# Kernel tuning notes

Hardware: AMD Instinct MI355X
Metric: run time of the kernel (lower is better)

The kernel has to match this reference:

```python
import jax, jax.numpy as jnp
import numpy as np
import math

D_MODEL = 1024
N_HEADS = 16
HEAD_DIM = D_MODEL // N_HEADS
B, S = 4, 4096


def setup_inputs() -> dict:
    key = jax.random.key(0)
    ks = jax.random.split(key, 8)
    # xavier-uniform-ish scale for square DxD matrices
    lim = math.sqrt(6.0 / (D_MODEL + D_MODEL))
    def W(k):
        return jax.random.uniform(k, (D_MODEL, D_MODEL), jnp.float32, -lim, lim)
    return {
        "x": jax.random.normal(ks[0], (B, S, D_MODEL), jnp.float32),
        "fractal_dim": jnp.float32(1.7),
        "Wq": W(ks[1]), "bq": jnp.zeros((D_MODEL,), jnp.float32),
        "Wk": W(ks[2]), "bk": jnp.zeros((D_MODEL,), jnp.float32),
        "Wv": W(ks[3]), "bv": jnp.zeros((D_MODEL,), jnp.float32),
        "Wo": W(ks[4]), "bo": jnp.zeros((D_MODEL,), jnp.float32),
        "alpha": jnp.float32(1.5),
        "frac_scale": jnp.float32(0.5),
    }


def reference(x, fractal_dim, Wq, bq, Wk, bk, Wv, bv, Wo, bo, alpha, frac_scale):
    b, s, d = x.shape
    h, hd = N_HEADS, HEAD_DIM
    residual = x

    adaptive_alpha = alpha + frac_scale * (fractal_dim - 1.5)

    q = (x @ Wq + bq).reshape(b, s, h, hd)
    k = (x @ Wk + bk).reshape(b, s, h, hd)
    v = (x @ Wv + bv).reshape(b, s, h, hd)

    # spectral filter over frequency axis (seq dim)
    freqs = jnp.fft.fftfreq(s).astype(x.dtype)  # [S]
    phase = adaptive_alpha * jnp.arctan(jnp.log(jnp.abs(freqs) + 1e-10))
    filt = jnp.exp(1j * phase)[None, :, None, None]  # [1,S,1,1] complex

    def spectral(t):
        tf = jnp.fft.fft(t, axis=1, norm="ortho") * filt
        return jnp.fft.ifft(tf, axis=1, norm="ortho").real

    q_t, k_t, v_t = spectral(q), spectral(k), spectral(v)

    # per-(token) dot product across head_dim -> logits over heads
    logits = jnp.einsum("bshd,bshd->bsh", q_t, k_t) / math.sqrt(hd)
    w = jax.nn.softmax(logits, axis=-1)  # softmax over heads
    attended = w[..., None] * v_t  # [B,S,H,Hd]

    # final inverse FFT of the (real) attended signal along seq dim
    attended_time = jnp.fft.ifft(attended.astype(jnp.complex64), axis=1, norm="ortho").real

    out = attended_time.reshape(b, s, d) @ Wo + bo
    return out + residual
```

## Files before the change

### kernel.cpp

```cpp
#include <hip/hip_runtime.h>

#define S      4096
#define DM     1024
#define NB     4
#define NH     16
#define HDIM   64
#define MTOT   (NB * S)
#define DS     ((long)DM * S)
#define MH     2304
#define KH     2112
#define KH2    2112
#define MEO    2048

typedef __attribute__((ext_vector_type(8))) short short8;
typedef __attribute__((ext_vector_type(4))) float f32x4;
typedef __attribute__((ext_vector_type(8))) unsigned short u16x8;
typedef __attribute__((ext_vector_type(4))) unsigned short u16x4;

__device__ __forceinline__ unsigned short f2bf(float f) {
  union { float f; unsigned u; } v; v.f = f;
  unsigned r = v.u + 0x7fffu + ((v.u >> 16) & 1u);
  return (unsigned short)(r >> 16);
}
__device__ __forceinline__ float bf2f(short h) {
  union { unsigned u; float f; } v; v.u = ((unsigned)(unsigned short)h) << 16;
  return v.f;
}

#define GLOAD(gp, lp) __builtin_amdgcn_global_load_lds( \
    (const __attribute__((address_space(1))) void*)(gp), \
    (__attribute__((address_space(3))) void*)(lp), 16, 0, 0)

#define SBAR() do { asm volatile("" ::: "memory"); __builtin_amdgcn_s_barrier(); \
                    asm volatile("" ::: "memory"); } while (0)
#define WAITL0() asm volatile("s_waitcnt lgkmcnt(0)" ::: "memory")

#define SWZ(o) ((o) ^ ((((o) >> 7) & 3) << 4))


__global__ void k_tables(const float* __restrict__ fd, const float* __restrict__ alpha,
                         const float* __restrict__ fsc,
                         float* __restrict__ cos_tab, float* __restrict__ c_arr) {
  int k = blockIdx.x * 256 + threadIdx.x;
  if (k >= S) return;
  float aa = alpha[0] + fsc[0] * (fd[0] - 1.5f);
  const float twopi = 6.28318530717958647692f;
  cos_tab[k] = cosf(twopi * ((float)k / (float)S));
  int kk = (k <= S / 2) ? k : (S - k);
  float af = (float)kk / (float)S;
  c_arr[k] = cosf(aa * atanf(logf(af + 1e-10f)));
}

__global__ void k_g(const float* __restrict__ cos_tab, const float* __restrict__ c_arr,
                    float* __restrict__ g) {
  __shared__ float sct[S];
  __shared__ float sc[S];
  __shared__ float red[16][17];
  for (int i = threadIdx.x; i < S; i += 256) { sct[i] = cos_tab[i]; sc[i] = c_arr[i]; }
  __syncthreads();
  int jl = threadIdx.x >> 4, r = threadIdx.x & 15;
  int j = blockIdx.x * 16 + jl;
  float acc = 0.f;
#pragma unroll 4
  for (int i = 0; i < 256; ++i) {
    int k = r + 16 * i;
    acc += sc[k] * sct[(j * k) & (S - 1)];
  }
  red[jl][r] = acc;
  __syncthreads();
  if (r == 0) {
    float s = 0.f;
#pragma unroll
    for (int i = 0; i < 16; ++i) s += red[jl][i];
    g[j] = s * (1.f / (float)S);
  }
}

__global__ void k_buildEO(const float* __restrict__ g, short* __restrict__ Ge) {
  long i8 = ((long)blockIdx.x * 256 + threadIdx.x) * 8;
  if (i8 >= (long)MEO * KH2) return;
  int n = (int)(i8 / KH2);
  int m = (int)(i8 % KH2);
  u16x8 ev, ov;
#pragma unroll
  for (int j = 0; j < 8; ++j) {
    int mm = m + j;
    float e, o;
    if (mm == 0)            { e = g[n]; o = 0.f; }
    else if (mm == 2048)    { e = g[(n + 2048) & (S - 1)]; o = 0.f; }
    else if (mm > 2048)     { e = 0.f; o = 0.f; }
    else {
      float a = g[(n - mm) & (S - 1)], b = g[(n + mm) & (S - 1)];
      e = 0.5f * (a + b); o = 0.5f * (a - b);
    }
    ev[j] = f2bf(e); ov[j] = f2bf(o);
  }
  *(u16x8*)(Ge + i8) = ev;
  *(u16x8*)(Ge + (long)MEO * KH2 + i8) = ov;
}

__global__ void k_foldT(const float* __restrict__ x, short* __restrict__ uv) {
  __shared__ float tp[64][65];
  __shared__ float tm[64][65];
  int m0 = blockIdx.x * 64, d0 = blockIdx.y * 64, b = blockIdx.z;
  int t = threadIdx.x;
  int r = t >> 4, c4 = (t & 15) * 4;
#pragma unroll
  for (int rr = 0; rr < 4; ++rr) {
    int m = m0 + r + rr * 16;
    float4 vp = *(const float4*)(x + ((long)(b * S + m)) * DM + d0 + c4);
    int ms = (S - m) & (S - 1);
    float4 vm = *(const float4*)(x + ((long)(b * S + ms)) * DM + d0 + c4);
    tp[r + rr * 16][c4 + 0] = vp.x; tp[r + rr * 16][c4 + 1] = vp.y;
    tp[r + rr * 16][c4 + 2] = vp.z; tp[r + rr * 16][c4 + 3] = vp.w;
    tm[r + rr * 16][c4 + 0] = vm.x; tm[r + rr * 16][c4 + 1] = vm.y;
    tm[r + rr * 16][c4 + 2] = vm.z; tm[r + rr * 16][c4 + 3] = vm.w;
  }
  __syncthreads();
  int m_loc = t & 63, dq = t >> 6;
#pragma unroll
  for (int i = 0; i < 16; ++i) {
    int d_loc = dq * 16 + i;
    int m = m0 + m_loc;
    float P = tp[m_loc][d_loc], M = tm[m_loc][d_loc];
    float u, v;
    if (m == 0 || m == 2048) { u = P; v = 0.f; }
    else if (m > 2048)       { u = 0.f; v = 0.f; }
    else                     { u = P + M; v = P - M; }
    long base = ((long)(b * DM + d0 + d_loc)) * KH2 + m;
    uv[base] = (short)f2bf(u);
    uv[base + (long)4 * DM * KH2] = (short)f2bf(v);
  }
}

__global__ void k_row2048(const float* __restrict__ g, const short* __restrict__ uv,
                          short* __restrict__ Xs) {
  __shared__ float red[256];
  int bd = blockIdx.x;
  int b = bd >> 10, d = bd & (DM - 1);
  const short* up = uv + ((long)(b * DM + d)) * KH2;
  int t = threadIdx.x;
  float acc = 0.f;
  for (int m = t; m <= 2048; m += 256)
    acc += g[2048 - m] * bf2f(up[m]);
  red[t] = acc;
  __syncthreads();
  for (int sh = 128; sh > 0; sh >>= 1) {
    if (t < sh) red[t] += red[t + sh];
    __syncthreads();
  }
  if (t == 0) Xs[((long)b * S + 2048) * DM + d] = (short)f2bf(red[0]);
}

__global__ void k_unfold(const short* __restrict__ AB, short* __restrict__ Xs) {
  long i8 = ((long)blockIdx.x * 256 + threadIdx.x) * 8;
  if (i8 >= (long)NB * MEO * DM) return;
  int b = (int)(i8 >> 21);
  long rr = i8 & ((1L << 21) - 1);
  int n = (int)(rr >> 10);
  int d = (int)(rr & (DM - 1));
  u16x8 av = *(const u16x8*)(AB + i8);
  u16x8 bv = *(const u16x8*)(AB + ((long)4 * MEO * DM) + i8);
  u16x8 sv, dv;
#pragma unroll
  for (int j = 0; j < 8; ++j) {
    float A = bf2f((short)av[j]), B = bf2f((short)bv[j]);
    sv[j] = f2bf(A + B);
    dv[j] = f2bf(A - B);
  }
  *(u16x8*)(Xs + ((long)b * S + n) * DM + d) = sv;
  if (n > 0)
    *(u16x8*)(Xs + ((long)b * S + (S - n)) * DM + d) = dv;
}

__global__ void k_buildM2(const float* __restrict__ cos_tab, short* __restrict__ Mc2) {
  long i8 = ((long)blockIdx.x * 256 + threadIdx.x) * 8;
  if (i8 >= (long)MH * KH) return;
  int n = (int)(i8 / KH);
  int m = (int)(i8 % KH);
  u16x8 mv;
#pragma unroll
  for (int j = 0; j < 8; ++j) {
    int mm = m + j;
    float vv = (mm <= 2048) ? cos_tab[(n * mm) & (S - 1)] * 0.015625f : 0.f;
    mv[j] = f2bf(vv);
  }
  *(u16x8*)(Mc2 + i8) = mv;
}

__global__ void k_transW(const float* __restrict__ W, short* __restrict__ WT) {
  __shared__ float tile[64][65];
  int k0 = blockIdx.x * 64, n0 = blockIdx.y * 64;
  int t = threadIdx.x;
  int r = t >> 4, c4 = (t & 15) * 4;
  const float* ip = W + (long)k0 * DM + n0;
#pragma unroll
  for (int rr = 0; rr < 4; ++rr) {
    float4 v = *(const float4*)(ip + (long)(r + rr * 16) * DM + c4);
    tile[r + rr * 16][c4 + 0] = v.x;
    tile[r + rr * 16][c4 + 1] = v.y;
    tile[r + rr * 16][c4 + 2] = v.z;
    tile[r + rr * 16][c4 + 3] = v.w;
  }
  __syncthreads();
  int k_loc = t & 63, nq = t >> 6;
  short* op = WT + (long)n0 * DM + k0;
#pragma unroll
  for (int i = 0; i < 16; ++i) {
    int n_loc = nq * 16 + i;
    op[(long)n_loc * DM + k_loc] = (short)f2bf(tile[k_loc][n_loc]);
  }
}

__global__ void k_logits(const short* __restrict__ Qt, const short* __restrict__ Kt,
                         float* __restrict__ logits) {
  int s = blockIdx.x * 256 + threadIdx.x;
  int h = blockIdx.y, b = blockIdx.z;
  const short* q = Qt + ((long)b * DM + h * HDIM) * S + s;
  const short* k = Kt + ((long)b * DM + h * HDIM) * S + s;
  float acc = 0.f;
#pragma unroll 8
  for (int j = 0; j < HDIM; ++j)
    acc += bf2f(q[(long)j * S]) * bf2f(k[(long)j * S]);
  logits[((long)b * NH + h) * S + s] = acc * 0.125f;
}

__global__ void k_softw(const float* __restrict__ logits, float* __restrict__ w) {
  int idx = blockIdx.x * 256 + threadIdx.x;
  if (idx >= NB * S) return;
  int b = idx >> 12, s = idx & (S - 1);
  const float* lp = logits + (long)b * NH * S + s;
  float v[NH];
  float m = -1e30f;
#pragma unroll
  for (int h = 0; h < NH; ++h) { v[h] = lp[(long)h * S]; m = fmaxf(m, v[h]); }
  float sum = 0.f;
#pragma unroll
  for (int h = 0; h < NH; ++h) { v[h] = expf(v[h] - m); sum += v[h]; }
  float inv = 1.f / sum;
  float* wp = w + (long)b * NH * S + s;
#pragma unroll
  for (int h = 0; h < NH; ++h) wp[(long)h * S] = v[h] * inv;
}

__global__ void k_att(short* vt, const float* __restrict__ wsm) {
  long i8 = ((long)blockIdx.x * 256 + threadIdx.x) * 8;
  if (i8 >= (long)NB * DS) return;
  int b = (int)(i8 >> 22);
  long r = i8 & (DS - 1);
  int d = (int)(r >> 12);
  int s = (int)(r & (S - 1));
  int h = d >> 6;
  const float* wp = wsm + ((long)b * NH + h) * S + s;
  u16x8 vv = *(const u16x8*)(vt + i8);
  u16x8 ov;
#pragma unroll
  for (int j = 0; j < 8; ++j) ov[j] = f2bf(wp[j] * bf2f((short)vv[j]));
  *(u16x8*)(vt + i8) = ov;
}

__global__ void k_fold(const short* __restrict__ att, short* __restrict__ A2t) {
  int m = blockIdx.x * 256 + threadIdx.x;
  if (m >= KH) return;
  int d = blockIdx.y, b = blockIdx.z;
  const short* ap = att + ((long)b * DM + d) * S;
  float v;
  if (m == 0) v = bf2f(ap[0]);
  else if (m < 2048) v = bf2f(ap[m]) + bf2f(ap[4096 - m]);
  else if (m == 2048) v = bf2f(ap[2048]);
  else v = 0.f;
  A2t[((long)b * DM + d) * KH + m] = (short)f2bf(v);
}

template <int EPI, int AMIR = 0, int ASEL = 0, int WALK = 0>
__global__ __launch_bounds__(512, 2) void gemm8(
    const short* __restrict__ A, const short* __restrict__ Bt,
    short* __restrict__ Cb, short* __restrict__ Cb2, short* __restrict__ Cb3,
    float* __restrict__ Cf,
    const float* __restrict__ bias, const float* __restrict__ bias2,
    const float* __restrict__ bias3,
    const float* __restrict__ bsc, const float* __restrict__ resid,
    int M, int N, int K, long aBatch, long bBatch, long cBatch) {
  __shared__ __align__(16) short As[2][2][256 * 32];
  __shared__ __align__(16) short Bs[2][2][256 * 32];

  const int gx = gridDim.x, gy = gridDim.y;
  const int nwg = gx * gy * gridDim.z;
  int lin = blockIdx.x + gx * (blockIdx.y + gy * blockIdx.z);
  int wg = lin;
  if ((nwg & 7) == 0) {
    const int cpx = nwg >> 3;
    wg = (lin & 7) * cpx + (lin >> 3);
  }
  const int NTN = N >> 8;
  const int NTM = M >> 8;
  int ntile, mtile, bz;
  if (WALK) {
    mtile = wg % NTM;
    const int rest = wg / NTM;
    ntile = rest % NTN;
    bz = rest / NTN;
  } else {
    ntile = wg % NTN;
    const int rest = wg / NTN;
    mtile = rest % NTM;
    bz = rest / NTM;
  }

  const short* Ag = ASEL ? (A + (long)(bz >> 2) * aBatch) : (A + (long)bz * aBatch);
  const short* Bg = Bt + (long)bz * bBatch;
  const int m0 = mtile << 8, n0 = ntile << 8;
  const int tid = threadIdx.x;
  const int lane = tid & 63;
  const int wid = tid >> 6;
  const int wm = wid >> 2, wn = wid & 3;

  f32x4 acc[8][4];
#pragma unroll
  for (int i = 0; i < 8; ++i)
#pragma unroll
    for (int j = 0; j < 4; ++j) acc[i][j] = (f32x4){0.f, 0.f, 0.f, 0.f};

  const int NT = K >> 6;
  auto stage = [&](int h) {
    const int tau = h >> 2, q = h & 3;
    const int buf = tau & 1, ks = q >> 1;
    short* ldsbase = (q & 1) ? &Bs[buf][ks][0] : &As[buf][ks][0];
    const short* gsrc = (q & 1) ? Bg : Ag;
    const int row0 = (q & 1) ? n0 : m0;
    const long k0 = (long)tau * 64 + ks * 32;
#pragma unroll
    for (int j = 0; j < 2; ++j) {
      const int o = tid * 16 + j * 8192;
      const int lo = SWZ(o);
      const int row = lo >> 6;
      const int cs = (lo & 63) >> 1;
      const short* gp;
      if (AMIR && !(q & 1)) {
        int grow = row0 + row;
        int b_ = grow >> 12, s_ = grow & (S - 1);
        int sm = (s_ <= 2048) ? s_ : (4096 - s_);
        gp = Ag + ((long)b_ * MH + sm) * K + k0 + cs;
      } else {
        gp = gsrc + (long)(row0 + row) * K + k0 + cs;
      }
      GLOAD(gp, (short*)((char*)ldsbase + o));
    }
  };

  for (int h = 0; h < 7; ++h) stage(h);
  asm volatile("s_waitcnt vmcnt(6)" ::: "memory");
  SBAR();

  short8 bf[4];
  for (int t = 0; t < NT; ++t) {
    const int buf = t & 1;
#pragma unroll
    for (int p = 0; p < 4; ++p) {
      const int ks = p >> 1, mh = p & 1;
      short8 af[4];
      {
        const short* Ah = &As[buf][ks][0];
        const int kb = (lane >> 4) * 16;
        const int r0 = wm * 128 + mh * 64 + (lane & 15);
#pragma unroll
        for (int i = 0; i < 4; ++i) {
          int byte = (r0 + i * 16) * 64 + kb;
          byte = SWZ(byte);
          af[i] = *(const short8*)((const char*)Ah + byte);
        }
        if (mh == 0) {
          const short* Bh = &Bs[buf][ks][0];
          const int c0 = wn * 64 + (lane & 15);
#pragma unroll
          for (int j = 0; j < 4; ++j) {
            int byte = (c0 + j * 16) * 64 + kb;
            byte = SWZ(byte);
            bf[j] = *(const short8*)((const char*)Bh + byte);
          }
        }
      }
      { const int h = 4 * t + p + 7; if (h < 4 * NT) stage(h); }
      SBAR();
      WAITL0();
      __builtin_amdgcn_s_setprio(1);
#pragma unroll
      for (int i = 0; i < 4; ++i)
#pragma unroll
        for (int j = 0; j < 4; ++j)
          acc[mh * 4 + i][j] = __builtin_amdgcn_mfma_f32_16x16x32_bf16(
              af[i], bf[j], acc[mh * 4 + i][j], 0, 0, 0);
      __builtin_amdgcn_s_setprio(0);
      if (p == 3) {
        if (t < NT - 2) {
          asm volatile("s_waitcnt vmcnt(6)" ::: "memory");
        } else if (t == NT - 2) {
          asm volatile("s_waitcnt vmcnt(0)" ::: "memory");
        }
      }
      SBAR();
    }
  }

  const int rl = (lane >> 4) << 2;
#pragma unroll
  for (int f = 0; f < 8; ++f) {
    const int rbase = m0 + wm * 128 + f * 16 + rl;
#pragma unroll
    for (int j = 0; j < 4; ++j) {
      const int col = n0 + wn * 64 + j * 16 + (lane & 15);
      f32x4 a = acc[f][j];
      if constexpr (EPI == 0) {
        short* cp = Cb + (long)bz * cBatch;
#pragma unroll
        for (int r = 0; r < 4; ++r)
          cp[(long)(rbase + r) * N + col] = (short)f2bf(a[r]);
      } else if constexpr (EPI == 1) {
        const float sc = bsc ? bsc[0] : 1.f;
        const int b_ = col >> 12;
        const int s_ = col & (S - 1);
#pragma unroll
        for (int r = 0; r < 4; ++r) {
          const int row = rbase + r;
          const int pidx = row >> 10;
          const int d = row & (DM - 1);
          short* Cp = (pidx == 0) ? Cb : ((pidx == 1) ? Cb2 : Cb3);
          const float* bp = (pidx == 0) ? bias : ((pidx == 1) ? bias2 : bias3);
          const float bi = bp ? bp[d] * sc : 0.f;
          Cp[((long)(b_ * DM + d)) * S + s_] = (short)f2bf(a[r] + bi);
        }
      } else {
        float bi = bias[col];
#pragma unroll
        for (int r = 0; r < 4; ++r) {
          long o = (long)(rbase + r) * N + col;
          Cf[o] = a[r] + bi + resid[o];
        }
      }
    }
  }
}

extern "C" void kernel_launch(void* const* d_in, const int* in_sizes, int n_in,
                              void* d_out, int out_size, void* d_ws, size_t ws_size,
                              hipStream_t stream) {
  const float* x     = (const float*)d_in[0];
  const float* fd    = (const float*)d_in[1];
  const float* Wq    = (const float*)d_in[2];
  const float* bq    = (const float*)d_in[3];
  const float* Wk    = (const float*)d_in[4];
  const float* bk    = (const float*)d_in[5];
  const float* Wv    = (const float*)d_in[6];
  const float* bv    = (const float*)d_in[7];
  const float* Wo    = (const float*)d_in[8];
  const float* bo    = (const float*)d_in[9];
  const float* alpha = (const float*)d_in[10];
  const float* fsc   = (const float*)d_in[11];
  float* out = (float*)d_out;

  char* wp = (char*)d_ws;
  auto alloc = [&](size_t bytes) {
    char* p = wp;
    wp += (bytes + 255) & ~(size_t)255;
    return p;
  };
  float* cos_tab = (float*)alloc(S * 4);
  float* c_arr   = (float*)alloc(S * 4);
  float* g       = (float*)alloc(S * 4);
  float* logits  = (float*)alloc((size_t)NB * NH * S * 4);
  float* wsm     = (float*)alloc((size_t)NB * NH * S * 4);
  short* WTcat = (short*)alloc((size_t)3 * DM * DM * 2);
  short* WoT   = (short*)alloc((size_t)DM * DM * 2);
  short* slotA = (short*)alloc((size_t)NB * DS * 2);
  short* slotB = (short*)alloc((size_t)NB * DS * 2);
  short* slotC = (short*)alloc((size_t)NB * DS * 2);

  short* uv  = (short*)d_out;
  short* QtT = (short*)d_out;
  short* KtT = (short*)d_out + (size_t)2 * DS;

  short* Ge  = slotB;
  short* ABout = slotA;
  short* Xs  = slotC;
  short* VtT = slotA;
  short* Mc2 = slotB;
  short* A2t = (short*)((char*)slotB + 10u * 1024 * 1024);
  short* att_half = slotC;

  dim3 blk(256), blk8(512);

  k_tables<<<dim3(S / 256), blk, 0, stream>>>(fd, alpha, fsc, cos_tab, c_arr);
  k_g<<<dim3(S / 16), blk, 0, stream>>>(cos_tab, c_arr, g);
  k_buildEO<<<dim3((unsigned)((long)MEO * KH2 / 8 / 256)), blk, 0, stream>>>(g, Ge);
  k_foldT<<<dim3(33, DM / 64, NB), blk, 0, stream>>>(x, uv);

  k_transW<<<dim3(16, 16), blk, 0, stream>>>(Wq, WTcat);
  k_transW<<<dim3(16, 16), blk, 0, stream>>>(Wk, WTcat + (size_t)DM * DM);
  k_transW<<<dim3(16, 16), blk, 0, stream>>>(Wv, WTcat + (size_t)2 * DM * DM);
  k_transW<<<dim3(16, 16), blk, 0, stream>>>(Wo, WoT);

  dim3 geo(DM / 256, MEO / 256, 8);
  gemm8<0, 0, 1><<<geo, blk8, 0, stream>>>(Ge, uv, ABout, nullptr, nullptr, nullptr,
                                           nullptr, nullptr, nullptr, nullptr, nullptr,
                                           MEO, DM, KH2,
                                           (long)MEO * KH2, (long)DM * KH2, (long)MEO * DM);
  k_row2048<<<dim3(NB * DM), blk, 0, stream>>>(g, uv, Xs);
  k_unfold<<<dim3((unsigned)((long)NB * MEO * DM / 8 / 256)), blk, 0, stream>>>(ABout, Xs);

  dim3 gqkv(MTOT / 256, 3 * DM / 256, 1);
  gemm8<1, 0, 0, 1><<<gqkv, blk8, 0, stream>>>(WTcat, Xs, QtT, KtT, VtT, nullptr,
                                               bq, bk, bv, c_arr, nullptr,
                                               3 * DM, MTOT, DM, 0, 0, 0);

  k_logits<<<dim3(S / 256, NH, NB), blk, 0, stream>>>(QtT, KtT, logits);
  k_softw<<<dim3(NB * S / 256), blk, 0, stream>>>(logits, wsm);
  k_att<<<dim3((unsigned)((long)NB * DS / 8 / 256)), blk, 0, stream>>>(VtT, wsm);

  k_fold<<<dim3(KH / 256 + 1, DM, NB), blk, 0, stream>>>(VtT, A2t);
  k_buildM2<<<dim3((unsigned)((long)MH * KH / 8 / 256)), blk, 0, stream>>>(cos_tab, Mc2);
  dim3 ghalf(DM / 256, MH / 256, NB);
  gemm8<0><<<ghalf, blk8, 0, stream>>>(Mc2, A2t, att_half, nullptr, nullptr, nullptr,
                                       nullptr, nullptr, nullptr, nullptr, nullptr,
                                       MH, DM, KH, 0, (long)DM * KH, (long)MH * DM);

  dim3 gproj(DM / 256, MTOT / 256, 1);
  gemm8<2, 1><<<gproj, blk8, 0, stream>>>(att_half, WoT, nullptr, nullptr, nullptr, out,
                                          bo, nullptr, nullptr, nullptr, x,
                                          MTOT, DM, DM, 0, 0, 0);
}
```

Baseline: 468.9 us.

## Fuse attention weighting into fold and stage QKV epilogue through LDS

Removes the standalone k_att pass by applying the softmax weights inside the fold kernel, which saves a full read and write of the V tensor. The QKV GEMM's operands are swapped so that tokens are the M dimension. A new epilogue writes the bf16 tile transposed into a swizzled shared buffer and then stores 16-byte coalesced rows into the [b,d,s] layout, replacing the previous scattered 2-byte stores. Shared memory is merged into one flat array so the epilogue can reuse it. The new epilogue drops the null check on the bias pointer, and the fused fold now reads the fp32 weights twice per output element.

```diff
diff --git a/kernel.cpp b/kernel.cpp
--- a/kernel.cpp
+++ b/kernel.cpp
@@ -243,31 +243,17 @@
   for (int h = 0; h < NH; ++h) wp[(long)h * S] = v[h] * inv;
 }
 
-__global__ void k_att(short* vt, const float* __restrict__ wsm) {
-  long i8 = ((long)blockIdx.x * 256 + threadIdx.x) * 8;
-  if (i8 >= (long)NB * DS) return;
-  int b = (int)(i8 >> 22);
-  long r = i8 & (DS - 1);
-  int d = (int)(r >> 12);
-  int s = (int)(r & (S - 1));
-  int h = d >> 6;
-  const float* wp = wsm + ((long)b * NH + h) * S + s;
-  u16x8 vv = *(const u16x8*)(vt + i8);
-  u16x8 ov;
-#pragma unroll
-  for (int j = 0; j < 8; ++j) ov[j] = f2bf(wp[j] * bf2f((short)vv[j]));
-  *(u16x8*)(vt + i8) = ov;
-}
-
-__global__ void k_fold(const short* __restrict__ att, short* __restrict__ A2t) {
+__global__ void k_attfold(const short* __restrict__ vt, const float* __restrict__ wsm,
+                          short* __restrict__ A2t) {
   int m = blockIdx.x * 256 + threadIdx.x;
   if (m >= KH) return;
   int d = blockIdx.y, b = blockIdx.z;
-  const short* ap = att + ((long)b * DM + d) * S;
+  const short* vp = vt + ((long)b * DM + d) * S;
+  const float* wp = wsm + ((long)b * NH + (d >> 6)) * S;
   float v;
-  if (m == 0) v = bf2f(ap[0]);
-  else if (m < 2048) v = bf2f(ap[m]) + bf2f(ap[4096 - m]);
-  else if (m == 2048) v = bf2f(ap[2048]);
+  if (m == 0) v = wp[0] * bf2f(vp[0]);
+  else if (m < 2048) v = wp[m] * bf2f(vp[m]) + wp[4096 - m] * bf2f(vp[4096 - m]);
+  else if (m == 2048) v = wp[2048] * bf2f(vp[2048]);
   else v = 0.f;
   A2t[((long)b * DM + d) * KH + m] = (short)f2bf(v);
 }
@@ -281,8 +267,9 @@
     const float* __restrict__ bias3,
     const float* __restrict__ bsc, const float* __restrict__ resid,
     int M, int N, int K, long aBatch, long bBatch, long cBatch) {
-  __shared__ __align__(16) short As[2][2][256 * 32];
-  __shared__ __align__(16) short Bs[2][2][256 * 32];
+  __shared__ __align__(16) short SH[65536];
+  auto Ab = [&](int buf, int ks) { return SH + (buf * 2 + ks) * 8192; };
+  auto Bb = [&](int buf, int ks) { return SH + 32768 + (buf * 2 + ks) * 8192; };
 
   const int gx = gridDim.x, gy = gridDim.y;
   const int nwg = gx * gy * gridDim.z;
@@ -325,7 +312,7 @@
   auto stage = [&](int h) {
     const int tau = h >> 2, q = h & 3;
     const int buf = tau & 1, ks = q >> 1;
-    short* ldsbase = (q & 1) ? &Bs[buf][ks][0] : &As[buf][ks][0];
+    short* ldsbase = (q & 1) ? Bb(buf, ks) : Ab(buf, ks);
     const short* gsrc = (q & 1) ? Bg : Ag;
     const int row0 = (q & 1) ? n0 : m0;
     const long k0 = (long)tau * 64 + ks * 32;
@@ -360,7 +347,7 @@
       const int ks = p >> 1, mh = p & 1;
       short8 af[4];
       {
-        const short* Ah = &As[buf][ks][0];
+        const short* Ah = Ab(buf, ks);
         const int kb = (lane >> 4) * 16;
         const int r0 = wm * 128 + mh * 64 + (lane & 15);
 #pragma unroll
@@ -370,7 +357,7 @@
           af[i] = *(const short8*)((const char*)Ah + byte);
         }
         if (mh == 0) {
-          const short* Bh = &Bs[buf][ks][0];
+          const short* Bh = Bb(buf, ks);
           const int c0 = wn * 64 + (lane & 15);
 #pragma unroll
           for (int j = 0; j < 4; ++j) {
@@ -403,6 +390,45 @@
   }
 
   const int rl = (lane >> 4) << 2;
+
+  if constexpr (EPI == 3) {
+    const int b_ = m0 >> 12;
+    const int s0 = m0 & (S - 1);
+    const int pidx = n0 >> 10;
+    const int d0 = n0 & (DM - 1);
+    const float* bp = (pidx == 0) ? bias : ((pidx == 1) ? bias2 : bias3);
+    short* Cp = (pidx == 0) ? Cb : ((pidx == 1) ? Cb2 : Cb3);
+    const float sc = bsc ? bsc[0] : 1.f;
+#pragma unroll
+    for (int f = 0; f < 8; ++f) {
+      const int lr0 = wm * 128 + f * 16 + rl;
+#pragma unroll
+      for (int j = 0; j < 4; ++j) {
+        const int lc = wn * 64 + j * 16 + (lane & 15);
+        const float bi = bp[d0 + lc] * sc;
+        f32x4 a = acc[f][j];
+        u16x4 pk;
+#pragma unroll
+        for (int r = 0; r < 4; ++r) pk[r] = f2bf(a[r] + bi);
+        int ad = lc * 512 + lr0 * 2;
+        ad ^= (lc & 7) << 4;
+        *(u16x4*)((char*)SH + ad) = pk;
+      }
+    }
+    __syncthreads();
+    const long gbase = ((long)(b_ * DM + d0)) * S + s0;
+#pragma unroll
+    for (int it = 0; it < 16; ++it) {
+      const int lc = wid * 32 + (it << 1) + (lane >> 5);
+      const int lr = (lane & 31) * 8;
+      int ad = lc * 512 + lr * 2;
+      ad ^= (lc & 7) << 4;
+      u16x8 vv = *(u16x8*)((char*)SH + ad);
+      *(u16x8*)(Cp + gbase + (long)lc * S + lr) = vv;
+    }
+    return;
+  }
+
 #pragma unroll
   for (int f = 0; f < 8; ++f) {
     const int rbase = m0 + wm * 128 + f * 16 + rl;
@@ -415,20 +441,6 @@
 #pragma unroll
         for (int r = 0; r < 4; ++r)
           cp[(long)(rbase + r) * N + col] = (short)f2bf(a[r]);
-      } else if constexpr (EPI == 1) {
-        const float sc = bsc ? bsc[0] : 1.f;
-        const int b_ = col >> 12;
-        const int s_ = col & (S - 1);
-#pragma unroll
-        for (int r = 0; r < 4; ++r) {
-          const int row = rbase + r;
-          const int pidx = row >> 10;
-          const int d = row & (DM - 1);
-          short* Cp = (pidx == 0) ? Cb : ((pidx == 1) ? Cb2 : Cb3);
-          const float* bp = (pidx == 0) ? bias : ((pidx == 1) ? bias2 : bias3);
-          const float bi = bp ? bp[d] * sc : 0.f;
-          Cp[((long)(b_ * DM + d)) * S + s_] = (short)f2bf(a[r] + bi);
-        }
       } else {
         float bi = bias[col];
 #pragma unroll
@@ -507,16 +519,15 @@
   k_row2048<<<dim3(NB * DM), blk, 0, stream>>>(g, uv, Xs);
   k_unfold<<<dim3((unsigned)((long)NB * MEO * DM / 8 / 256)), blk, 0, stream>>>(ABout, Xs);
 
-  dim3 gqkv(MTOT / 256, 3 * DM / 256, 1);
-  gemm8<1, 0, 0, 1><<<gqkv, blk8, 0, stream>>>(WTcat, Xs, QtT, KtT, VtT, nullptr,
-                                               bq, bk, bv, c_arr, nullptr,
-                                               3 * DM, MTOT, DM, 0, 0, 0);
+  dim3 gqkv(3 * DM / 256, MTOT / 256, 1);
+  gemm8<3><<<gqkv, blk8, 0, stream>>>(Xs, WTcat, QtT, KtT, VtT, nullptr,
+                                      bq, bk, bv, c_arr, nullptr,
+                                      MTOT, 3 * DM, DM, 0, 0, 0);
 
   k_logits<<<dim3(S / 256, NH, NB), blk, 0, stream>>>(QtT, KtT, logits);
   k_softw<<<dim3(NB * S / 256), blk, 0, stream>>>(logits, wsm);
-  k_att<<<dim3((unsigned)((long)NB * DS / 8 / 256)), blk, 0, stream>>>(VtT, wsm);
-
-  k_fold<<<dim3(KH / 256 + 1, DM, NB), blk, 0, stream>>>(VtT, A2t);
+  k_attfold<<<dim3(KH / 256 + 1, DM, NB), blk, 0, stream>>>(VtT, wsm, A2t);
+
   k_buildM2<<<dim3((unsigned)((long)MH * KH / 8 / 256)), blk, 0, stream>>>(cos_tab, Mc2);
   dim3 ghalf(DM / 256, MH / 256, NB);
   gemm8<0><<<ghalf, blk8, 0, stream>>>(Mc2, A2t, att_half, nullptr, nullptr, nullptr,
```

Measured after the change: 413.8 us. 11.8% less time.
